# Kernel optimization log

Measured on AMD Instinct MI355X. Metric: run time of the kernel, lower is better.

Reference implementation:

```python
import jax, jax.numpy as jnp
import numpy as np

N, E, F_IN, HID, HEADS, LAYERS, CLASSES = 50000, 800000, 128, 96, 4, 3, 8
C = HID // HEADS
NEG_SLOPE = 0.2
BN_EPS = 1e-5


def setup_inputs() -> dict:
    key = jax.random.key(0)
    ks = jax.random.split(key, 32)
    inp = {}
    inp['x'] = jax.random.normal(ks[0], (N, F_IN), dtype=jnp.float32)
    inp['edge_index'] = jax.random.randint(ks[1], (2, E), 0, N, dtype=jnp.int32)
    dims = [F_IN, HID, HID]
    for i in range(LAYERS):
        inp[f'W{i}'] = jax.random.normal(ks[2 + 5 * i], (dims[i], HID), dtype=jnp.float32) * 0.1
        inp[f'as{i}'] = jax.random.normal(ks[3 + 5 * i], (HEADS, C), dtype=jnp.float32) * 0.1
        inp[f'ad{i}'] = jax.random.normal(ks[4 + 5 * i], (HEADS, C), dtype=jnp.float32) * 0.1
        inp[f'b{i}'] = jnp.zeros((HID,), dtype=jnp.float32)
        inp[f'g{i}'] = jnp.ones((HID,), dtype=jnp.float32)
        inp[f'bt{i}'] = jnp.zeros((HID,), dtype=jnp.float32)
    inp['fcW'] = jax.random.normal(ks[30], (HID, CLASSES), dtype=jnp.float32) * 0.1
    inp['fcb'] = jnp.zeros((CLASSES,), dtype=jnp.float32)
    return inp


def _gat_layer(x, W, a_src, a_dst, bias, src, dst):
    # x: [N, Fin] -> h: [N, H, C]
    h = (x @ W).reshape(N, HEADS, C)
    alpha_s = jnp.einsum('nhc,hc->nh', h, a_src)  # [N, H]
    alpha_d = jnp.einsum('nhc,hc->nh', h, a_dst)
    e = jax.nn.leaky_relu(alpha_s[src] + alpha_d[dst], NEG_SLOPE)  # [E', H]
    # softmax over incoming edges per destination node (per head)
    m = jax.lax.stop_gradient(jax.ops.segment_max(e, dst, num_segments=N))
    ex = jnp.exp(e - m[dst])
    den = jax.ops.segment_sum(ex, dst, num_segments=N)
    alpha = ex / (den[dst] + 1e-16)  # [E', H]
    out = jax.ops.segment_sum(h[src] * alpha[..., None], dst, num_segments=N)  # [N,H,C]
    return out.reshape(N, HID) + bias


def _bn(x, gamma, beta):
    mu = x.mean(axis=0)
    var = x.var(axis=0)
    return gamma * (x - mu) * jax.lax.rsqrt(var + BN_EPS) + beta


def reference(x, edge_index, W0, as0, ad0, b0, g0, bt0, W1, as1, ad1, b1, g1, bt1,
              W2, as2, ad2, b2, g2, bt2, fcW, fcb):
    loop = jnp.arange(N, dtype=edge_index.dtype)
    src = jnp.concatenate([edge_index[0], loop])  # GATConv adds self-loops
    dst = jnp.concatenate([edge_index[1], loop])
    params = [(W0, as0, ad0, b0, g0, bt0), (W1, as1, ad1, b1, g1, bt1),
              (W2, as2, ad2, b2, g2, bt2)]
    h = x
    for (W, a_s, a_d, b, g, bt) in params:
        h = _gat_layer(h, W, a_s, a_d, b, src, dst)
        h = jax.nn.elu(_bn(h, g, bt))
    return h @ fcW + fcb
```

## Files before the change

### kernel.cpp

```cpp
#include <hip/hip_runtime.h>
#include <hip/hip_bf16.h>

#define NN 50000
#define EE 800000
#define FIN 128
#define HID 96
#define HEADS 4
#define CDIM 24
#define NEG_SLOPE 0.2f
#define BN_EPS 1e-5f
#define NPART 196

__device__ __forceinline__ float lrelu(float x) { return x > 0.f ? x : NEG_SLOPE * x; }
__device__ __forceinline__ float elu(float x) { return x > 0.f ? x : expm1f(x); }
__device__ __forceinline__ float sel4(float4 v, int h) {
    return (h & 2) ? ((h & 1) ? v.w : v.z) : ((h & 1) ? v.y : v.x);
}
__device__ __forceinline__ unsigned fenc(float f) {
    unsigned b = __float_as_uint(f);
    return (b & 0x80000000u) ? ~b : (b | 0x80000000u);
}
__device__ __forceinline__ float fdec(unsigned u) {
    return (u & 0x80000000u) ? __uint_as_float(u & 0x7FFFFFFFu) : __uint_as_float(~u);
}

__global__ void count_deg_kernel(const int* __restrict__ dst, int* __restrict__ cnt) {
    int i = blockIdx.x * 256 + threadIdx.x;
    if (i < EE) atomicAdd(&cnt[dst[i]], 1);
}

__global__ __launch_bounds__(256) void scan_part_kernel(const int* __restrict__ cnt,
                                                        int* __restrict__ part) {
    int t = threadIdx.x;
    int i = blockIdx.x * 256 + t;
    int v = (i < NN) ? cnt[i] : 0;
#pragma unroll
    for (int off = 1; off < 64; off <<= 1) v += __shfl_xor(v, off);
    __shared__ int ws[4];
    if ((t & 63) == 0) ws[t >> 6] = v;
    __syncthreads();
    if (t == 0) part[blockIdx.x] = ws[0] + ws[1] + ws[2] + ws[3];
}

__global__ __launch_bounds__(256) void scan_partsum_kernel(int* __restrict__ part) {
    int t = threadIdx.x;
    int lane = t & 63, wv = t >> 6;
    int v = (t < NPART) ? part[t] : 0;
    int x = v;
#pragma unroll
    for (int off = 1; off < 64; off <<= 1) {
        int y = __shfl_up(x, off);
        if (lane >= off) x += y;
    }
    __shared__ int wsum[4];
    if (lane == 63) wsum[wv] = x;
    __syncthreads();
    int wb = 0;
    for (int i = 0; i < wv; i++) wb += wsum[i];
    if (t < NPART) part[t] = wb + x - v;
}

__global__ __launch_bounds__(256) void scan_final_kernel(const int* __restrict__ cnt,
                                                         const int* __restrict__ part,
                                                         int* __restrict__ row_off) {
    int t = threadIdx.x;
    int i = blockIdx.x * 256 + t;
    int lane = t & 63, wv = t >> 6;
    int v = (i < NN) ? cnt[i] : 0;
    int x = v;
#pragma unroll
    for (int off = 1; off < 64; off <<= 1) {
        int y = __shfl_up(x, off);
        if (lane >= off) x += y;
    }
    __shared__ int wsum[4];
    if (lane == 63) wsum[wv] = x;
    __syncthreads();
    int wb = 0;
    for (int j = 0; j < wv; j++) wb += wsum[j];
    if (i < NN) row_off[i] = part[blockIdx.x] + wb + x - v;
    if (i == NN) row_off[NN] = EE;
}

__global__ void scatter_kernel(const int* __restrict__ src, const int* __restrict__ dst,
                               const int* __restrict__ row_off, int* __restrict__ cnt,
                               int* __restrict__ col_src) {
    int i = blockIdx.x * 256 + threadIdx.x;
    if (i < EE) {
        int d = dst[i];
        int pos = atomicSub(&cnt[d], 1) - 1;
        col_src[row_off[d] + pos] = src[i];
    }
}

template <int K, bool BN>
__global__ __launch_bounds__(256) void gemm_kernel(const float* __restrict__ X,
                                                   const float* __restrict__ W,
                                                   const float* __restrict__ a_s,
                                                   const float* __restrict__ a_d,
                                                   const float* __restrict__ ss,
                                                   float* __restrict__ H,
                                                   float* __restrict__ As,
                                                   float* __restrict__ Ad,
                                                   unsigned* __restrict__ amaxU) {
    const int KC = 32;
    __shared__ float Ws[KC * 96];
    __shared__ float Xs[32][KC + 4];
    __shared__ unsigned amx[4];
    int t = threadIdx.x;
    if (t < 4) amx[t] = 0u;
    int row0 = blockIdx.x * 32;
    int r = t >> 4;
    int i16 = t & 15;
    int c0 = i16 * 6;
    int slr = t >> 3;
    int sq = t & 7;
    float accA[6] = {0.f, 0.f, 0.f, 0.f, 0.f, 0.f};
    float accB[6] = {0.f, 0.f, 0.f, 0.f, 0.f, 0.f};
    for (int k0 = 0; k0 < K; k0 += KC) {
        for (int i = t; i < KC * 24; i += 256)
            ((float4*)Ws)[i] = ((const float4*)(W + (size_t)k0 * 96))[i];
        {
            float4 v = make_float4(0.f, 0.f, 0.f, 0.f);
            if (row0 + slr < NN) {
                v = *(const float4*)(X + (size_t)(row0 + slr) * K + k0 + sq * 4);
                if (BN) {
                    int f = k0 + sq * 4;
                    v.x = elu(v.x * ss[f + 0] + ss[96 + f + 0]);
                    v.y = elu(v.y * ss[f + 1] + ss[96 + f + 1]);
                    v.z = elu(v.z * ss[f + 2] + ss[96 + f + 2]);
                    v.w = elu(v.w * ss[f + 3] + ss[96 + f + 3]);
                }
            }
            *(float4*)(&Xs[slr][sq * 4]) = v;
        }
        __syncthreads();
#pragma unroll
        for (int k = 0; k < KC; k++) {
            float va = Xs[r][k];
            float vb = Xs[r + 16][k];
            const float* wr = &Ws[k * 96 + c0];
#pragma unroll
            for (int j = 0; j < 6; j++) {
                accA[j] += va * wr[j];
                accB[j] += vb * wr[j];
            }
        }
        __syncthreads();
    }
    int gA = row0 + r, gB = row0 + 16 + r;
    float* outA = H + (size_t)gA * 96 + c0;
#pragma unroll
    for (int j = 0; j < 6; j++) outA[j] = accA[j];
    if (gB < NN) {
        float* outB = H + (size_t)gB * 96 + c0;
#pragma unroll
        for (int j = 0; j < 6; j++) outB[j] = accB[j];
    }

    int hh = i16 >> 2;
    const float* asl = a_s + c0;
    const float* adl = a_d + c0;
    float psA = 0.f, pdA = 0.f, psB = 0.f, pdB = 0.f;
#pragma unroll
    for (int j = 0; j < 6; j++) {
        psA += accA[j] * asl[j];
        pdA += accA[j] * adl[j];
        psB += accB[j] * asl[j];
        pdB += accB[j] * adl[j];
    }
    psA += __shfl_xor(psA, 1); psA += __shfl_xor(psA, 2);
    pdA += __shfl_xor(pdA, 1); pdA += __shfl_xor(pdA, 2);
    psB += __shfl_xor(psB, 1); psB += __shfl_xor(psB, 2);
    pdB += __shfl_xor(pdB, 1); pdB += __shfl_xor(pdB, 2);
    if ((t & 3) == 0) {
        As[gA * 4 + hh] = psA;
        Ad[gA * 4 + hh] = pdA;
        if (gB < NN) {
            As[gB * 4 + hh] = psB;
            Ad[gB * 4 + hh] = pdB;
        }
    }
    float psMax = (gB < NN) ? fmaxf(psA, psB) : psA;
    psMax = fmaxf(psMax, __shfl_xor(psMax, 16));
    psMax = fmaxf(psMax, __shfl_xor(psMax, 32));
    if ((t & 51) == 0) atomicMax(&amx[hh], fenc(psMax));
    __syncthreads();
    if (t < 4) atomicMax(&amaxU[t], amx[t]);
}

__global__ __launch_bounds__(256) void agg_kernel(const float* __restrict__ H,
                                                  const float* __restrict__ As,
                                                  const float* __restrict__ Ad,
                                                  const unsigned* __restrict__ Mu,
                                                  const int* __restrict__ row_off,
                                                  const int* __restrict__ col_src,
                                                  const float* __restrict__ bias,
                                                  float* __restrict__ out) {
    int wave = threadIdx.x >> 6;
    int lane = threadIdx.x & 63;
    int n = blockIdx.x * 4 + wave;
    if (n >= NN) return;
    int f1 = lane;
    int f2 = lane + 64;
    int h1 = f1 / CDIM;
    int h2 = f2 / CDIM;
    const float4* As4 = (const float4*)As;
    float4 ad = ((const float4*)Ad)[n];
    float4 M = make_float4(fdec(Mu[0]), fdec(Mu[1]), fdec(Mu[2]), fdec(Mu[3]));
    float ad1 = sel4(ad, h1);
    float ad2 = sel4(ad, h2);
    float m1 = lrelu(sel4(M, h1) + ad1);
    float m2 = lrelu(sel4(M, h2) + ad2);
    int beg = row_off[n], end = row_off[n + 1];

    float s1 = 0.f, s2 = 0.f, acc1 = 0.f, acc2 = 0.f;
    {
        float4 a = As4[n];
        float p = __expf(lrelu(sel4(a, h1) + ad1) - m1);
        s1 += p;
        acc1 += p * H[(size_t)n * 96 + f1];
        if (lane < 32) {
            float q = __expf(lrelu(sel4(a, h2) + ad2) - m2);
            s2 += q;
            acc2 += q * H[(size_t)n * 96 + f2];
        }
    }
    int e = beg;
    for (; e + 4 <= end; e += 4) {
        int sa = col_src[e], sb = col_src[e + 1], sc = col_src[e + 2], sd = col_src[e + 3];
        float4 a0 = As4[sa], a1 = As4[sb], a2 = As4[sc], a3 = As4[sd];
        float g0 = H[(size_t)sa * 96 + f1];
        float g1 = H[(size_t)sb * 96 + f1];
        float g2 = H[(size_t)sc * 96 + f1];
        float g3 = H[(size_t)sd * 96 + f1];
        float p0 = __expf(lrelu(sel4(a0, h1) + ad1) - m1);
        float p1 = __expf(lrelu(sel4(a1, h1) + ad1) - m1);
        float p2 = __expf(lrelu(sel4(a2, h1) + ad1) - m1);
        float p3 = __expf(lrelu(sel4(a3, h1) + ad1) - m1);
        s1 += p0; s1 += p1; s1 += p2; s1 += p3;
        acc1 += p0 * g0; acc1 += p1 * g1; acc1 += p2 * g2; acc1 += p3 * g3;
        if (lane < 32) {
            float u0 = H[(size_t)sa * 96 + f2];
            float u1 = H[(size_t)sb * 96 + f2];
            float u2 = H[(size_t)sc * 96 + f2];
            float u3 = H[(size_t)sd * 96 + f2];
            float q0 = __expf(lrelu(sel4(a0, h2) + ad2) - m2);
            float q1 = __expf(lrelu(sel4(a1, h2) + ad2) - m2);
            float q2 = __expf(lrelu(sel4(a2, h2) + ad2) - m2);
            float q3 = __expf(lrelu(sel4(a3, h2) + ad2) - m2);
            s2 += q0; s2 += q1; s2 += q2; s2 += q3;
            acc2 += q0 * u0; acc2 += q1 * u1; acc2 += q2 * u2; acc2 += q3 * u3;
        }
    }
    for (; e < end; e++) {
        int s = col_src[e];
        float4 a = As4[s];
        float p = __expf(lrelu(sel4(a, h1) + ad1) - m1);
        s1 += p;
        acc1 += p * H[(size_t)s * 96 + f1];
        if (lane < 32) {
            float q = __expf(lrelu(sel4(a, h2) + ad2) - m2);
            s2 += q;
            acc2 += q * H[(size_t)s * 96 + f2];
        }
    }
    out[(size_t)n * 96 + f1] = acc1 / (s1 + 1e-16f) + bias[f1];
    if (lane < 32) out[(size_t)n * 96 + f2] = acc2 / (s2 + 1e-16f) + bias[f2];
}

__global__ __launch_bounds__(192) void bn_stats_kernel(const float* __restrict__ Y,
                                                       float* __restrict__ accum) {
    int t = threadIdx.x;
    float4 s = {0.f, 0.f, 0.f, 0.f}, q = {0.f, 0.f, 0.f, 0.f};
    for (int i4 = blockIdx.x * 192 + t; i4 < NN * 24; i4 += 512 * 192) {
        float4 v = ((const float4*)Y)[i4];
        s.x += v.x; s.y += v.y; s.z += v.z; s.w += v.w;
        q.x += v.x * v.x; q.y += v.y * v.y; q.z += v.z * v.z; q.w += v.w * v.w;
    }
    __shared__ float4 ls[192], lq[192];
    ls[t] = s;
    lq[t] = q;
    __syncthreads();
    if (t < 24) {
        float4 S = ls[t], Q = lq[t];
        for (int i = 1; i < 8; i++) {
            float4 a = ls[t + 24 * i], b = lq[t + 24 * i];
            S.x += a.x; S.y += a.y; S.z += a.z; S.w += a.w;
            Q.x += b.x; Q.y += b.y; Q.z += b.z; Q.w += b.w;
        }
        int f = t * 4;
        atomicAdd(&accum[f + 0], S.x); atomicAdd(&accum[f + 1], S.y);
        atomicAdd(&accum[f + 2], S.z); atomicAdd(&accum[f + 3], S.w);
        atomicAdd(&accum[96 + f + 0], Q.x); atomicAdd(&accum[96 + f + 1], Q.y);
        atomicAdd(&accum[96 + f + 2], Q.z); atomicAdd(&accum[96 + f + 3], Q.w);
    }
}

__global__ void bn_final_kernel(const float* __restrict__ accum, const float* __restrict__ g,
                                const float* __restrict__ bt, float* __restrict__ ss) {
    int f = threadIdx.x;
    if (f >= 96) return;
    float mean = accum[f] * (1.0f / NN);
    float var = accum[96 + f] * (1.0f / NN) - mean * mean;
    float sc = g[f] * rsqrtf(var + BN_EPS);
    ss[f] = sc;
    ss[96 + f] = bt[f] - mean * sc;
}

__global__ __launch_bounds__(256) void fc_kernel(const float* __restrict__ Y,
                                                 const float* __restrict__ ss,
                                                 const float* __restrict__ W,
                                                 const float* __restrict__ b,
                                                 float* __restrict__ out) {
    __shared__ float w[96 * 8];
    __shared__ float yl[32][100];
    __shared__ float bb[8];
    int t = threadIdx.x;
    for (int i = t; i < 768; i += 256) w[i] = W[i];
    if (t < 8) bb[t] = b[t];
    int row0 = blockIdx.x * 32;
    for (int i = t; i < 768; i += 256) {
        int lr = i / 24, q = i % 24;
        float4 v = make_float4(0.f, 0.f, 0.f, 0.f);
        if (row0 + lr < NN) {
            v = *(const float4*)(Y + (size_t)(row0 + lr) * 96 + q * 4);
            int f = q * 4;
            v.x = elu(v.x * ss[f + 0] + ss[96 + f + 0]);
            v.y = elu(v.y * ss[f + 1] + ss[96 + f + 1]);
            v.z = elu(v.z * ss[f + 2] + ss[96 + f + 2]);
            v.w = elu(v.w * ss[f + 3] + ss[96 + f + 3]);
        }
        *(float4*)(&yl[lr][q * 4]) = v;
    }
    __syncthreads();
    int ln = t >> 3;
    int cl = t & 7;
    int n = row0 + ln;
    if (n >= NN) return;
    float acc = bb[cl];
#pragma unroll 8
    for (int k = 0; k < 96; k++) acc += yl[ln][k] * w[k * 8 + cl];
    out[(size_t)n * 8 + cl] = acc;
}

extern "C" void kernel_launch(void* const* d_in, const int* in_sizes, int n_in,
                              void* d_out, int out_size, void* d_ws, size_t ws_size,
                              hipStream_t stream) {
    const float* x = (const float*)d_in[0];
    const int* ei = (const int*)d_in[1];
    const int* srcE = ei;
    const int* dstE = ei + EE;
    const float* Wl[3] = {(const float*)d_in[2], (const float*)d_in[8], (const float*)d_in[14]};
    const float* asl[3] = {(const float*)d_in[3], (const float*)d_in[9], (const float*)d_in[15]};
    const float* adl[3] = {(const float*)d_in[4], (const float*)d_in[10], (const float*)d_in[16]};
    const float* bl[3] = {(const float*)d_in[5], (const float*)d_in[11], (const float*)d_in[17]};
    const float* gl[3] = {(const float*)d_in[6], (const float*)d_in[12], (const float*)d_in[18]};
    const float* btl[3] = {(const float*)d_in[7], (const float*)d_in[13], (const float*)d_in[19]};
    const float* fcW = (const float*)d_in[20];
    const float* fcb = (const float*)d_in[21];
    float* out = (float*)d_out;

    char* w = (char*)d_ws;
    float* bufA = (float*)w;            w += (size_t)NN * 96 * 4;
    float* bufB = (float*)w;            w += (size_t)NN * 96 * 4;
    float* alpha_s = (float*)w;         w += (size_t)NN * 4 * 4;
    float* alpha_d = (float*)w;         w += (size_t)NN * 4 * 4;
    float* bn_accum = (float*)w;        w += 192 * 4;
    unsigned* amaxU = (unsigned*)w;     w += 4 * 4;
    float* bn_ss = (float*)w;           w += 192 * 4;
    int* row_off = (int*)w;             w += (size_t)(NN + 4) * 4;
    int* cnt = (int*)w;                 w += (size_t)NN * 4;
    int* spart = (int*)w;               w += 256 * 4;
    int* col_src = (int*)w;             w += (size_t)EE * 4;

    hipMemsetAsync(cnt, 0, (size_t)NN * 4, stream);
    count_deg_kernel<<<(EE + 255) / 256, 256, 0, stream>>>(dstE, cnt);
    scan_part_kernel<<<NPART, 256, 0, stream>>>(cnt, spart);
    scan_partsum_kernel<<<1, 256, 0, stream>>>(spart);
    scan_final_kernel<<<NPART, 256, 0, stream>>>(cnt, spart, row_off);
    scatter_kernel<<<(EE + 255) / 256, 256, 0, stream>>>(srcE, dstE, row_off, cnt, col_src);

    for (int l = 0; l < 3; l++) {
        hipMemsetAsync(bn_accum, 0, 196 * 4, stream);
        if (l == 0)
            gemm_kernel<128, false><<<(NN + 31) / 32, 256, 0, stream>>>(
                x, Wl[l], asl[l], adl[l], nullptr, bufA, alpha_s, alpha_d, amaxU);
        else
            gemm_kernel<96, true><<<(NN + 31) / 32, 256, 0, stream>>>(
                bufB, Wl[l], asl[l], adl[l], bn_ss, bufA, alpha_s, alpha_d, amaxU);
        agg_kernel<<<(NN + 3) / 4, 256, 0, stream>>>(bufA, alpha_s, alpha_d, amaxU, row_off,
                                                     col_src, bl[l], bufB);
        bn_stats_kernel<<<512, 192, 0, stream>>>(bufB, bn_accum);
        bn_final_kernel<<<1, 128, 0, stream>>>(bn_accum, gl[l], btl[l], bn_ss);
    }
    fc_kernel<<<(NN + 31) / 32, 256, 0, stream>>>(bufB, bn_ss, fcW, fcb, out);
}
```

Baseline: 710.3 us.

## Fold BN finalize and scan into consumers, retile GEMM, vectorize aggregation

Removes the separate partial-sum scan and BN finalize kernels plus per-layer memsets by computing scan prefixes and BN scale/shift inside consumer kernels and double-buffering accumulators zeroed by other kernels. GEMM tiles grow to 64 rows with 12 columns per thread and float4 LDS/global accesses. Aggregation uses 48 lanes each handling a float2 instead of a divergent two-feature scheme. This trades a few redundant per-block computations for fewer launches and better memory access.

```diff
diff --git a/kernel.cpp b/kernel.cpp
--- a/kernel.cpp
+++ b/kernel.cpp
@@ -1,15 +1,13 @@
 #include <hip/hip_runtime.h>
-#include <hip/hip_bf16.h>
 
 #define NN 50000
 #define EE 800000
-#define FIN 128
 #define HID 96
-#define HEADS 4
 #define CDIM 24
 #define NEG_SLOPE 0.2f
 #define BN_EPS 1e-5f
 #define NPART 196
+#define ACST 200
 
 __device__ __forceinline__ float lrelu(float x) { return x > 0.f ? x : NEG_SLOPE * x; }
 __device__ __forceinline__ float elu(float x) { return x > 0.f ? x : expm1f(x); }
@@ -24,8 +22,10 @@
     return (u & 0x80000000u) ? __uint_as_float(u & 0x7FFFFFFFu) : __uint_as_float(~u);
 }
 
-__global__ void count_deg_kernel(const int* __restrict__ dst, int* __restrict__ cnt) {
+__global__ void count_deg_kernel(const int* __restrict__ dst, int* __restrict__ cnt,
+                                 float* __restrict__ accumBase) {
     int i = blockIdx.x * 256 + threadIdx.x;
+    if (blockIdx.x == 0 && threadIdx.x < 2 * ACST) accumBase[threadIdx.x] = 0.f;
     if (i < EE) atomicAdd(&cnt[dst[i]], 1);
 }
 
@@ -42,28 +42,20 @@
     if (t == 0) part[blockIdx.x] = ws[0] + ws[1] + ws[2] + ws[3];
 }
 
-__global__ __launch_bounds__(256) void scan_partsum_kernel(int* __restrict__ part) {
-    int t = threadIdx.x;
-    int lane = t & 63, wv = t >> 6;
-    int v = (t < NPART) ? part[t] : 0;
-    int x = v;
-#pragma unroll
-    for (int off = 1; off < 64; off <<= 1) {
-        int y = __shfl_up(x, off);
-        if (lane >= off) x += y;
-    }
-    __shared__ int wsum[4];
-    if (lane == 63) wsum[wv] = x;
-    __syncthreads();
-    int wb = 0;
-    for (int i = 0; i < wv; i++) wb += wsum[i];
-    if (t < NPART) part[t] = wb + x - v;
-}
-
 __global__ __launch_bounds__(256) void scan_final_kernel(const int* __restrict__ cnt,
                                                          const int* __restrict__ part,
                                                          int* __restrict__ row_off) {
     int t = threadIdx.x;
+    __shared__ int pre_s;
+    __shared__ int wsum[4];
+    if (t < 64) {
+        int acc = 0;
+        for (int j = t; j < blockIdx.x; j += 64) acc += part[j];
+#pragma unroll
+        for (int off = 1; off < 64; off <<= 1) acc += __shfl_xor(acc, off);
+        if (t == 0) pre_s = acc;
+    }
+    __syncthreads();
     int i = blockIdx.x * 256 + t;
     int lane = t & 63, wv = t >> 6;
     int v = (i < NN) ? cnt[i] : 0;
@@ -73,12 +65,11 @@
         int y = __shfl_up(x, off);
         if (lane >= off) x += y;
     }
-    __shared__ int wsum[4];
     if (lane == 63) wsum[wv] = x;
     __syncthreads();
     int wb = 0;
     for (int j = 0; j < wv; j++) wb += wsum[j];
-    if (i < NN) row_off[i] = part[blockIdx.x] + wb + x - v;
+    if (i < NN) row_off[i] = pre_s + wb + x - v;
     if (i == NN) row_off[NN] = EE;
 }
 
@@ -98,93 +89,103 @@
                                                    const float* __restrict__ W,
                                                    const float* __restrict__ a_s,
                                                    const float* __restrict__ a_d,
-                                                   const float* __restrict__ ss,
+                                                   const float* __restrict__ accumPrev,
+                                                   const float* __restrict__ gam,
+                                                   const float* __restrict__ bet,
                                                    float* __restrict__ H,
                                                    float* __restrict__ As,
                                                    float* __restrict__ Ad,
                                                    unsigned* __restrict__ amaxU) {
     const int KC = 32;
     __shared__ float Ws[KC * 96];
-    __shared__ float Xs[32][KC + 4];
+    __shared__ float Xs[64][KC + 4];
+    __shared__ float ssl[192];
     __shared__ unsigned amx[4];
     int t = threadIdx.x;
     if (t < 4) amx[t] = 0u;
-    int row0 = blockIdx.x * 32;
-    int r = t >> 4;
-    int i16 = t & 15;
-    int c0 = i16 * 6;
-    int slr = t >> 3;
-    int sq = t & 7;
-    float accA[6] = {0.f, 0.f, 0.f, 0.f, 0.f, 0.f};
-    float accB[6] = {0.f, 0.f, 0.f, 0.f, 0.f, 0.f};
+    if (BN && t < 96) {
+        float mean = accumPrev[t] * (1.0f / NN);
+        float var = accumPrev[96 + t] * (1.0f / NN) - mean * mean;
+        float sc = gam[t] * rsqrtf(var + BN_EPS);
+        ssl[t] = sc;
+        ssl[96 + t] = bet[t] - mean * sc;
+    }
+    if (BN) __syncthreads();
+    int row0 = blockIdx.x * 64;
+    int grp = t & 7, rs = t >> 3;
+    int c0 = grp * 12;
+    float accA[12], accB[12];
+#pragma unroll
+    for (int j = 0; j < 12; j++) { accA[j] = 0.f; accB[j] = 0.f; }
     for (int k0 = 0; k0 < K; k0 += KC) {
         for (int i = t; i < KC * 24; i += 256)
             ((float4*)Ws)[i] = ((const float4*)(W + (size_t)k0 * 96))[i];
-        {
+        for (int i = t; i < 64 * (KC / 4); i += 256) {
+            int lr = i >> 3, q = i & 7;
             float4 v = make_float4(0.f, 0.f, 0.f, 0.f);
-            if (row0 + slr < NN) {
-                v = *(const float4*)(X + (size_t)(row0 + slr) * K + k0 + sq * 4);
+            if (row0 + lr < NN) {
+                v = *(const float4*)(X + (size_t)(row0 + lr) * K + k0 + q * 4);
                 if (BN) {
-                    int f = k0 + sq * 4;
-                    v.x = elu(v.x * ss[f + 0] + ss[96 + f + 0]);
-                    v.y = elu(v.y * ss[f + 1] + ss[96 + f + 1]);
-                    v.z = elu(v.z * ss[f + 2] + ss[96 + f + 2]);
-                    v.w = elu(v.w * ss[f + 3] + ss[96 + f + 3]);
+                    int f = k0 + q * 4;
+                    v.x = elu(v.x * ssl[f + 0] + ssl[96 + f + 0]);
+                    v.y = elu(v.y * ssl[f + 1] + ssl[96 + f + 1]);
+                    v.z = elu(v.z * ssl[f + 2] + ssl[96 + f + 2]);
+                    v.w = elu(v.w * ssl[f + 3] + ssl[96 + f + 3]);
                 }
             }
-            *(float4*)(&Xs[slr][sq * 4]) = v;
+            *(float4*)(&Xs[lr][q * 4]) = v;
         }
         __syncthreads();
 #pragma unroll
         for (int k = 0; k < KC; k++) {
-            float va = Xs[r][k];
-            float vb = Xs[r + 16][k];
-            const float* wr = &Ws[k * 96 + c0];
-#pragma unroll
-            for (int j = 0; j < 6; j++) {
-                accA[j] += va * wr[j];
-                accB[j] += vb * wr[j];
-            }
+            float va = Xs[rs][k];
+            float vb = Xs[rs + 32][k];
+            const float4* wr = (const float4*)(&Ws[k * 96 + c0]);
+            float4 w0 = wr[0], w1 = wr[1], w2 = wr[2];
+            accA[0] += va * w0.x; accA[1] += va * w0.y; accA[2] += va * w0.z; accA[3] += va * w0.w;
+            accA[4] += va * w1.x; accA[5] += va * w1.y; accA[6] += va * w1.z; accA[7] += va * w1.w;
+            accA[8] += va * w2.x; accA[9] += va * w2.y; accA[10] += va * w2.z; accA[11] += va * w2.w;
+            accB[0] += vb * w0.x; accB[1] += vb * w0.y; accB[2] += vb * w0.z; accB[3] += vb * w0.w;
+            accB[4] += vb * w1.x; accB[5] += vb * w1.y; accB[6] += vb * w1.z; accB[7] += vb * w1.w;
+            accB[8] += vb * w2.x; accB[9] += vb * w2.y; accB[10] += vb * w2.z; accB[11] += vb * w2.w;
         }
         __syncthreads();
     }
-    int gA = row0 + r, gB = row0 + 16 + r;
-    float* outA = H + (size_t)gA * 96 + c0;
-#pragma unroll
-    for (int j = 0; j < 6; j++) outA[j] = accA[j];
-    if (gB < NN) {
-        float* outB = H + (size_t)gB * 96 + c0;
-#pragma unroll
-        for (int j = 0; j < 6; j++) outB[j] = accB[j];
-    }
-
-    int hh = i16 >> 2;
-    const float* asl = a_s + c0;
-    const float* adl = a_d + c0;
+    int gA = row0 + rs, gB = row0 + 32 + rs;
+    bool vA = gA < NN, vB = gB < NN;
+    if (vA) {
+        float* o = H + (size_t)gA * 96 + c0;
+        *(float4*)(o + 0) = make_float4(accA[0], accA[1], accA[2], accA[3]);
+        *(float4*)(o + 4) = make_float4(accA[4], accA[5], accA[6], accA[7]);
+        *(float4*)(o + 8) = make_float4(accA[8], accA[9], accA[10], accA[11]);
+    }
+    if (vB) {
+        float* o = H + (size_t)gB * 96 + c0;
+        *(float4*)(o + 0) = make_float4(accB[0], accB[1], accB[2], accB[3]);
+        *(float4*)(o + 4) = make_float4(accB[4], accB[5], accB[6], accB[7]);
+        *(float4*)(o + 8) = make_float4(accB[8], accB[9], accB[10], accB[11]);
+    }
     float psA = 0.f, pdA = 0.f, psB = 0.f, pdB = 0.f;
 #pragma unroll
-    for (int j = 0; j < 6; j++) {
-        psA += accA[j] * asl[j];
-        pdA += accA[j] * adl[j];
-        psB += accB[j] * asl[j];
-        pdB += accB[j] * adl[j];
-    }
-    psA += __shfl_xor(psA, 1); psA += __shfl_xor(psA, 2);
-    pdA += __shfl_xor(pdA, 1); pdA += __shfl_xor(pdA, 2);
-    psB += __shfl_xor(psB, 1); psB += __shfl_xor(psB, 2);
-    pdB += __shfl_xor(pdB, 1); pdB += __shfl_xor(pdB, 2);
-    if ((t & 3) == 0) {
-        As[gA * 4 + hh] = psA;
-        Ad[gA * 4 + hh] = pdA;
-        if (gB < NN) {
-            As[gB * 4 + hh] = psB;
-            Ad[gB * 4 + hh] = pdB;
-        }
-    }
-    float psMax = (gB < NN) ? fmaxf(psA, psB) : psA;
-    psMax = fmaxf(psMax, __shfl_xor(psMax, 16));
-    psMax = fmaxf(psMax, __shfl_xor(psMax, 32));
-    if ((t & 51) == 0) atomicMax(&amx[hh], fenc(psMax));
+    for (int j = 0; j < 12; j++) {
+        float av = a_s[c0 + j], dv = a_d[c0 + j];
+        psA += accA[j] * av; pdA += accA[j] * dv;
+        psB += accB[j] * av; pdB += accB[j] * dv;
+    }
+    psA += __shfl_xor(psA, 1); pdA += __shfl_xor(pdA, 1);
+    psB += __shfl_xor(psB, 1); pdB += __shfl_xor(pdB, 1);
+    int hh = grp >> 1;
+    if ((t & 1) == 0) {
+        if (vA) { As[gA * 4 + hh] = psA; Ad[gA * 4 + hh] = pdA; }
+        if (vB) { As[gB * 4 + hh] = psB; Ad[gB * 4 + hh] = pdB; }
+    }
+    float pm = vA ? psA : -3.4e38f;
+    if (vB) pm = fmaxf(pm, psB);
+    pm = fmaxf(pm, __shfl_xor(pm, 1));
+    pm = fmaxf(pm, __shfl_xor(pm, 8));
+    pm = fmaxf(pm, __shfl_xor(pm, 16));
+    pm = fmaxf(pm, __shfl_xor(pm, 32));
+    if ((t & 57) == 0) atomicMax(&amx[hh], fenc(pm));
     __syncthreads();
     if (t < 4) atomicMax(&amaxU[t], amx[t]);
 }
@@ -200,78 +201,64 @@
     int wave = threadIdx.x >> 6;
     int lane = threadIdx.x & 63;
     int n = blockIdx.x * 4 + wave;
-    if (n >= NN) return;
-    int f1 = lane;
-    int f2 = lane + 64;
-    int h1 = f1 / CDIM;
-    int h2 = f2 / CDIM;
+    if (lane >= 48) return;
+    int h = lane / 12;
     const float4* As4 = (const float4*)As;
-    float4 ad = ((const float4*)Ad)[n];
-    float4 M = make_float4(fdec(Mu[0]), fdec(Mu[1]), fdec(Mu[2]), fdec(Mu[3]));
-    float ad1 = sel4(ad, h1);
-    float ad2 = sel4(ad, h2);
-    float m1 = lrelu(sel4(M, h1) + ad1);
-    float m2 = lrelu(sel4(M, h2) + ad2);
+    const float2* H2 = (const float2*)H;
+    float4 adv = ((const float4*)Ad)[n];
+    float ad_h = sel4(adv, h);
+    float m = lrelu(fdec(Mu[h]) + ad_h);
     int beg = row_off[n], end = row_off[n + 1];
 
-    float s1 = 0.f, s2 = 0.f, acc1 = 0.f, acc2 = 0.f;
+    float s1 = 0.f;
+    float2 acc = {0.f, 0.f};
     {
         float4 a = As4[n];
-        float p = __expf(lrelu(sel4(a, h1) + ad1) - m1);
+        float p = __expf(lrelu(sel4(a, h) + ad_h) - m);
+        float2 hv = H2[(size_t)n * 48 + lane];
         s1 += p;
-        acc1 += p * H[(size_t)n * 96 + f1];
-        if (lane < 32) {
-            float q = __expf(lrelu(sel4(a, h2) + ad2) - m2);
-            s2 += q;
-            acc2 += q * H[(size_t)n * 96 + f2];
-        }
+        acc.x += p * hv.x; acc.y += p * hv.y;
     }
     int e = beg;
     for (; e + 4 <= end; e += 4) {
         int sa = col_src[e], sb = col_src[e + 1], sc = col_src[e + 2], sd = col_src[e + 3];
         float4 a0 = As4[sa], a1 = As4[sb], a2 = As4[sc], a3 = As4[sd];
-        float g0 = H[(size_t)sa * 96 + f1];
-        float g1 = H[(size_t)sb * 96 + f1];
-        float g2 = H[(size_t)sc * 96 + f1];
-        float g3 = H[(size_t)sd * 96 + f1];
-        float p0 = __expf(lrelu(sel4(a0, h1) + ad1) - m1);
-        float p1 = __expf(lrelu(sel4(a1, h1) + ad1) - m1);
-        float p2 = __expf(lrelu(sel4(a2, h1) + ad1) - m1);
-        float p3 = __expf(lrelu(sel4(a3, h1) + ad1) - m1);
+        float2 h0 = H2[(size_t)sa * 48 + lane];
+        float2 h1 = H2[(size_t)sb * 48 + lane];
+        float2 h2v = H2[(size_t)sc * 48 + lane];
+        float2 h3 = H2[(size_t)sd * 48 + lane];
+        float p0 = __expf(lrelu(sel4(a0, h) + ad_h) - m);
+        float p1 = __expf(lrelu(sel4(a1, h) + ad_h) - m);
+        float p2 = __expf(lrelu(sel4(a2, h) + ad_h) - m);
+        float p3 = __expf(lrelu(sel4(a3, h) + ad_h) - m);
         s1 += p0; s1 += p1; s1 += p2; s1 += p3;
-        acc1 += p0 * g0; acc1 += p1 * g1; acc1 += p2 * g2; acc1 += p3 * g3;
-        if (lane < 32) {
-            float u0 = H[(size_t)sa * 96 + f2];
-            float u1 = H[(size_t)sb * 96 + f2];
-            float u2 = H[(size_t)sc * 96 + f2];
-            float u3 = H[(size_t)sd * 96 + f2];
-            float q0 = __expf(lrelu(sel4(a0, h2) + ad2) - m2);
-            float q1 = __expf(lrelu(sel4(a1, h2) + ad2) - m2);
-            float q2 = __expf(lrelu(sel4(a2, h2) + ad2) - m2);
-            float q3 = __expf(lrelu(sel4(a3, h2) + ad2) - m2);
-            s2 += q0; s2 += q1; s2 += q2; s2 += q3;
-            acc2 += q0 * u0; acc2 += q1 * u1; acc2 += q2 * u2; acc2 += q3 * u3;
-        }
+        acc.x += p0 * h0.x; acc.y += p0 * h0.y;
+        acc.x += p1 * h1.x; acc.y += p1 * h1.y;
+        acc.x += p2 * h2v.x; acc.y += p2 * h2v.y;
+        acc.x += p3 * h3.x; acc.y += p3 * h3.y;
     }
     for (; e < end; e++) {
         int s = col_src[e];
         float4 a = As4[s];
-        float p = __expf(lrelu(sel4(a, h1) + ad1) - m1);
+        float p = __expf(lrelu(sel4(a, h) + ad_h) - m);
+        float2 hv = H2[(size_t)s * 48 + lane];
         s1 += p;
-        acc1 += p * H[(size_t)s * 96 + f1];
-        if (lane < 32) {
-            float q = __expf(lrelu(sel4(a, h2) + ad2) - m2);
-            s2 += q;
-            acc2 += q * H[(size_t)s * 96 + f2];
-        }
-    }
-    out[(size_t)n * 96 + f1] = acc1 / (s1 + 1e-16f) + bias[f1];
-    if (lane < 32) out[(size_t)n * 96 + f2] = acc2 / (s2 + 1e-16f) + bias[f2];
+        acc.x += p * hv.x; acc.y += p * hv.y;
+    }
+    float inv = 1.f / (s1 + 1e-16f);
+    float2 b2 = ((const float2*)bias)[lane];
+    float2 o;
+    o.x = acc.x * inv + b2.x;
+    o.y = acc.y * inv + b2.y;
+    ((float2*)out)[(size_t)n * 48 + lane] = o;
 }
 
 __global__ __launch_bounds__(192) void bn_stats_kernel(const float* __restrict__ Y,
-                                                       float* __restrict__ accum) {
-    int t = threadIdx.x;
+                                                       float* __restrict__ accum,
+                                                       float* __restrict__ other) {
+    int t = threadIdx.x;
+    int zi = blockIdx.x * 192 + t;
+    if (zi < ACST) other[zi] = 0.f;
     float4 s = {0.f, 0.f, 0.f, 0.f}, q = {0.f, 0.f, 0.f, 0.f};
     for (int i4 = blockIdx.x * 192 + t; i4 < NN * 24; i4 += 512 * 192) {
         float4 v = ((const float4*)Y)[i4];
@@ -297,28 +284,28 @@
     }
 }
 
-__global__ void bn_final_kernel(const float* __restrict__ accum, const float* __restrict__ g,
-                                const float* __restrict__ bt, float* __restrict__ ss) {
-    int f = threadIdx.x;
-    if (f >= 96) return;
-    float mean = accum[f] * (1.0f / NN);
-    float var = accum[96 + f] * (1.0f / NN) - mean * mean;
-    float sc = g[f] * rsqrtf(var + BN_EPS);
-    ss[f] = sc;
-    ss[96 + f] = bt[f] - mean * sc;
-}
-
 __global__ __launch_bounds__(256) void fc_kernel(const float* __restrict__ Y,
-                                                 const float* __restrict__ ss,
+                                                 const float* __restrict__ accumPrev,
+                                                 const float* __restrict__ gam,
+                                                 const float* __restrict__ bet,
                                                  const float* __restrict__ W,
                                                  const float* __restrict__ b,
                                                  float* __restrict__ out) {
     __shared__ float w[96 * 8];
     __shared__ float yl[32][100];
+    __shared__ float ssl[192];
     __shared__ float bb[8];
     int t = threadIdx.x;
+    if (t < 96) {
+        float mean = accumPrev[t] * (1.0f / NN);
+        float var = accumPrev[96 + t] * (1.0f / NN) - mean * mean;
+        float sc = gam[t] * rsqrtf(var + BN_EPS);
+        ssl[t] = sc;
+        ssl[96 + t] = bet[t] - mean * sc;
+    }
     for (int i = t; i < 768; i += 256) w[i] = W[i];
     if (t < 8) bb[t] = b[t];
+    __syncthreads();
     int row0 = blockIdx.x * 32;
     for (int i = t; i < 768; i += 256) {
         int lr = i / 24, q = i % 24;
@@ -326,10 +313,10 @@
         if (row0 + lr < NN) {
             v = *(const float4*)(Y + (size_t)(row0 + lr) * 96 + q * 4);
             int f = q * 4;
-            v.x = elu(v.x * ss[f + 0] + ss[96 + f + 0]);
-            v.y = elu(v.y * ss[f + 1] + ss[96 + f + 1]);
-            v.z = elu(v.z * ss[f + 2] + ss[96 + f + 2]);
-            v.w = elu(v.w * ss[f + 3] + ss[96 + f + 3]);
+            v.x = elu(v.x * ssl[f + 0] + ssl[96 + f + 0]);
+            v.y = elu(v.y * ssl[f + 1] + ssl[96 + f + 1]);
+            v.z = elu(v.z * ssl[f + 2] + ssl[96 + f + 2]);
+            v.w = elu(v.w * ssl[f + 3] + ssl[96 + f + 3]);
         }
         *(float4*)(&yl[lr][q * 4]) = v;
     }
@@ -362,37 +349,38 @@
     float* out = (float*)d_out;
 
     char* w = (char*)d_ws;
-    float* bufA = (float*)w;            w += (size_t)NN * 96 * 4;
-    float* bufB = (float*)w;            w += (size_t)NN * 96 * 4;
-    float* alpha_s = (float*)w;         w += (size_t)NN * 4 * 4;
-    float* alpha_d = (float*)w;         w += (size_t)NN * 4 * 4;
-    float* bn_accum = (float*)w;        w += 192 * 4;
-    unsigned* amaxU = (unsigned*)w;     w += 4 * 4;
-    float* bn_ss = (float*)w;           w += 192 * 4;
-    int* row_off = (int*)w;             w += (size_t)(NN + 4) * 4;
-    int* cnt = (int*)w;                 w += (size_t)NN * 4;
-    int* spart = (int*)w;               w += 256 * 4;
-    int* col_src = (int*)w;             w += (size_t)EE * 4;
+    float* bufA = (float*)w;        w += (size_t)NN * 96 * 4;
+    float* bufB = (float*)w;        w += (size_t)NN * 96 * 4;
+    float* alpha_s = (float*)w;     w += (size_t)NN * 4 * 4;
+    float* alpha_d = (float*)w;     w += (size_t)NN * 4 * 4;
+    float* accumBase = (float*)w;   w += 2 * ACST * 4;
+    int* row_off = (int*)w;         w += (size_t)(NN + 4) * 4;
+    int* cnt = (int*)w;             w += (size_t)NN * 4;
+    int* spart = (int*)w;           w += 256 * 4;
+    int* col_src = (int*)w;         w += (size_t)EE * 4;
+
+    float* slot[2] = {accumBase, accumBase + ACST};
+    unsigned* amax[2] = {(unsigned*)(accumBase + 192), (unsigned*)(accumBase + ACST + 192)};
 
     hipMemsetAsync(cnt, 0, (size_t)NN * 4, stream);
-    count_deg_kernel<<<(EE + 255) / 256, 256, 0, stream>>>(dstE, cnt);
+    count_deg_kernel<<<(EE + 255) / 256, 256, 0, stream>>>(dstE, cnt, accumBase);
     scan_part_kernel<<<NPART, 256, 0, stream>>>(cnt, spart);
-    scan_partsum_kernel<<<1, 256, 0, stream>>>(spart);
     scan_final_kernel<<<NPART, 256, 0, stream>>>(cnt, spart, row_off);
     scatter_kernel<<<(EE + 255) / 256, 256, 0, stream>>>(srcE, dstE, row_off, cnt, col_src);
 
     for (int l = 0; l < 3; l++) {
-        hipMemsetAsync(bn_accum, 0, 196 * 4, stream);
+        int sl = l & 1, so = (l + 1) & 1;
         if (l == 0)
-            gemm_kernel<128, false><<<(NN + 31) / 32, 256, 0, stream>>>(
-                x, Wl[l], asl[l], adl[l], nullptr, bufA, alpha_s, alpha_d, amaxU);
+            gemm_kernel<128, false><<<(NN + 63) / 64, 256, 0, stream>>>(
+                x, Wl[0], asl[0], adl[0], nullptr, nullptr, nullptr,
+                bufA, alpha_s, alpha_d, amax[0]);
         else
-            gemm_kernel<96, true><<<(NN + 31) / 32, 256, 0, stream>>>(
-                bufB, Wl[l], asl[l], adl[l], bn_ss, bufA, alpha_s, alpha_d, amaxU);
-        agg_kernel<<<(NN + 3) / 4, 256, 0, stream>>>(bufA, alpha_s, alpha_d, amaxU, row_off,
-                                                     col_src, bl[l], bufB);
-        bn_stats_kernel<<<512, 192, 0, stream>>>(bufB, bn_accum);
-        bn_final_kernel<<<1, 128, 0, stream>>>(bn_accum, gl[l], btl[l], bn_ss);
-    }
-    fc_kernel<<<(NN + 31) / 32, 256, 0, stream>>>(bufB, bn_ss, fcW, fcb, out);
-}
+            gemm_kernel<96, true><<<(NN + 63) / 64, 256, 0, stream>>>(
+                bufB, Wl[l], asl[l], adl[l], slot[so], gl[l - 1], btl[l - 1],
+                bufA, alpha_s, alpha_d, amax[sl]);
+        agg_kernel<<<(NN + 3) / 4, 256, 0, stream>>>(bufA, alpha_s, alpha_d, amax[sl],
+                                                     row_off, col_src, bl[l], bufB);
+        bn_stats_kernel<<<512, 192, 0, stream>>>(bufB, slot[sl], slot[so]);
+    }
+    fc_kernel<<<(NN + 31) / 32, 256, 0, stream>>>(bufB, slot[0], gl[2], btl[2], fcW, fcb, out);
+}
```

After: 663.8 us. 1.07x faster.
